# Optimization experiments

Hardware: AMD Instinct MI355X
Metric: run time of the kernel (lower is better)

The kernel has to match this reference:

```python
import jax, jax.numpy as jnp
import numpy as np

N = 50000          # nodes
E = 1_600_000      # edges (avg degree 32)
D_IN = 128
D_H = 128
D_OUT = 64
L = 3              # GATv2 layers
NEG_SLOPE = 0.2    # PyG GATv2Conv default negative_slope


def setup_inputs() -> dict:
    key = jax.random.key(0)
    ks = jax.random.split(key, 12)
    s = 0.05
    x = jax.random.normal(ks[0], (N, D_IN), jnp.float32)
    edge_index = jax.random.randint(ks[1], (2, E), 0, N, jnp.int32)
    # stacked per-layer GATv2 params (input_dim == hidden_dim so all layers match)
    Wl = jax.random.normal(ks[2], (L, D_H, D_H), jnp.float32) * s   # lin_l weights
    bl = jnp.zeros((L, D_H), jnp.float32)
    Wr = jax.random.normal(ks[3], (L, D_H, D_H), jnp.float32) * s   # lin_r weights
    br = jnp.zeros((L, D_H), jnp.float32)
    att = jax.random.normal(ks[4], (L, D_H), jnp.float32) * s       # attention vector a
    bias = jnp.zeros((L, D_H), jnp.float32)                          # post-aggregation bias
    # post_mp MLP head
    W1 = jax.random.normal(ks[5], (D_H, D_H), jnp.float32) * s
    b1 = jnp.zeros((D_H,), jnp.float32)
    W2 = jax.random.normal(ks[6], (D_OUT, D_H), jnp.float32) * s
    b2 = jnp.zeros((D_OUT,), jnp.float32)
    return {"x": x, "edge_index": edge_index, "Wl": Wl, "bl": bl, "Wr": Wr,
            "br": br, "att": att, "bias": bias, "W1": W1, "b1": b1, "W2": W2, "b2": b2}


def _gatv2_layer(x, src, dst, Wl, bl, Wr, br, att, bias):
    # lin_l on source features, lin_r on destination features (heads=1)
    xl = x @ Wl.T + bl                                   # [N, D_H]
    xr = x @ Wr.T + br                                   # [N, D_H]
    e = jax.nn.leaky_relu(xl[src] + xr[dst], NEG_SLOPE)  # [E, D_H]
    logits = e @ att                                     # [E]
    # segment softmax over incoming edges of each destination node
    m = jax.ops.segment_max(logits, dst, num_segments=N)
    ex = jnp.exp(logits - m[dst])
    denom = jax.ops.segment_sum(ex, dst, num_segments=N)
    alpha = ex / denom[dst]                              # [E]
    msg = xl[src] * alpha[:, None]                       # [E, D_H]
    out = jax.ops.segment_sum(msg, dst, num_segments=N)  # [N, D_H]
    return out + bias


def reference(x, edge_index, Wl, bl, Wr, br, att, bias, W1, b1, W2, b2):
    src, dst = edge_index[0], edge_index[1]
    for i in range(L):
        x = _gatv2_layer(x, src, dst, Wl[i], bl[i], Wr[i], br[i], att[i], bias[i])
        x = jax.nn.relu(x)  # dropout is identity in eval mode
    h = x @ W1.T + b1
    return h @ W2.T + b2  # return_embedding=True -> raw output
```

## Files before the change

kernel.cpp:

```cpp
#include <hip/hip_runtime.h>
#include <hip/hip_bf16.h>

#define NN 50000
#define EE 1600000
#define DH 128
#define DOUT 64
#define NEG 0.2f
#define NBK 256
#define CHUNK 4096

typedef short bf16x8 __attribute__((ext_vector_type(8)));
typedef float f32x4 __attribute__((ext_vector_type(4)));


__global__ __launch_bounds__(256) void k_bhist(const int* __restrict__ dst,
                                               int* __restrict__ bucket_hist) {
    __shared__ int lh[NBK];
    lh[threadIdx.x] = 0;
    __syncthreads();
    const int e0 = blockIdx.x * CHUNK;
    #pragma unroll
    for (int k = 0; k < CHUNK / 256; k++) {
        int e = e0 + k * 256 + threadIdx.x;
        if (e < EE) atomicAdd(&lh[((unsigned)dst[e]) >> 8], 1);
    }
    __syncthreads();
    int c = lh[threadIdx.x];
    if (c) atomicAdd(&bucket_hist[threadIdx.x], c);
}

__global__ __launch_bounds__(256) void k_scan_bucket(const int* __restrict__ bucket_hist,
                                                     int* __restrict__ bucket_base,
                                                     int* __restrict__ bucket_cursor) {
    __shared__ int tmp[NBK];
    int t = threadIdx.x;
    int v = bucket_hist[t];
    tmp[t] = v;
    __syncthreads();
    #pragma unroll
    for (int off = 1; off < NBK; off <<= 1) {
        int tt = (t >= off) ? tmp[t - off] : 0;
        __syncthreads();
        tmp[t] += tt;
        __syncthreads();
    }
    bucket_base[t] = tmp[t] - v;
    bucket_cursor[t] = tmp[t] - v;
}

__global__ __launch_bounds__(256) void k_scatter(const int* __restrict__ src,
                                                 const int* __restrict__ dst,
                                                 int* __restrict__ bucket_cursor,
                                                 uint2* __restrict__ pairs) {
    __shared__ int lh[NBK];
    __shared__ int lbase[NBK];
    lh[threadIdx.x] = 0;
    __syncthreads();
    const int e0 = blockIdx.x * CHUNK;
    int dl[CHUNK / 256];
    #pragma unroll
    for (int k = 0; k < CHUNK / 256; k++) {
        int e = e0 + k * 256 + threadIdx.x;
        dl[k] = (e < EE) ? dst[e] : -1;
        if (dl[k] >= 0) atomicAdd(&lh[((unsigned)dl[k]) >> 8], 1);
    }
    __syncthreads();
    int c = lh[threadIdx.x];
    lbase[threadIdx.x] = c ? atomicAdd(&bucket_cursor[threadIdx.x], c) : 0;
    __syncthreads();
    lh[threadIdx.x] = 0;
    __syncthreads();
    #pragma unroll
    for (int k = 0; k < CHUNK / 256; k++) {
        int e = e0 + k * 256 + threadIdx.x;
        if (dl[k] >= 0) {
            int b = ((unsigned)dl[k]) >> 8;
            int loc = atomicAdd(&lh[b], 1);
            pairs[lbase[b] + loc] = make_uint2((unsigned)src[e], (unsigned)dl[k]);
        }
    }
}

__global__ __launch_bounds__(256) void k_bucket(const uint2* __restrict__ pairs,
                                                const int* __restrict__ bucket_base,
                                                const int* __restrict__ bucket_hist,
                                                int* __restrict__ csr_off,
                                                int* __restrict__ prow,
                                                int* __restrict__ deg) {
    __shared__ int cnt[256];
    __shared__ int sbase[256];
    __shared__ int scn[256];
    __shared__ int cur[256];
    const int b = blockIdx.x;
    const int t = threadIdx.x;
    const int pstart = bucket_base[b];
    const int pcnt = bucket_hist[b];

    cnt[t] = 0;
    cur[t] = 0;
    __syncthreads();
    for (int i = t; i < pcnt; i += 256)
        atomicAdd(&cnt[pairs[pstart + i].y & 255u], 1);
    __syncthreads();

    const int d = cnt[t];
    const int padded = (d + 7) & ~7;
    scn[t] = padded;
    __syncthreads();
    #pragma unroll
    for (int off = 1; off < 256; off <<= 1) {
        int v = (t >= off) ? scn[t - off] : 0;
        __syncthreads();
        scn[t] += v;
        __syncthreads();
    }
    const int mybase = scn[t] - padded;
    sbase[t] = mybase;
    const int cb = pstart + b * 2048;
    const int node = b * 256 + t;
    if (node < NN) {
        prow[node] = cb + mybase;
        deg[node] = d;
    }
    __syncthreads();

    for (int i = t; i < pcnt; i += 256) {
        uint2 pr = pairs[pstart + i];
        int ln = (int)(pr.y & 255u);
        int pos = atomicAdd(&cur[ln], 1);
        csr_off[cb + sbase[ln] + pos] = (int)(pr.x << 8);
    }
    __syncthreads();

    for (int p = d; p < padded; p++) csr_off[cb + mybase + p] = 0;
}


static __device__ __forceinline__ unsigned int f2bf(float f) {
    unsigned int u = __float_as_uint(f);
    return (u + 0x7fffu + ((u >> 16) & 1u)) >> 16;
}
static __device__ __forceinline__ unsigned int pack2bf(float lo, float hi) {
    return f2bf(lo) | (f2bf(hi) << 16);
}


template <int BN>
__global__ __launch_bounds__(256) void k_mfma(const float* __restrict__ X,
                                              const float* __restrict__ W0,
                                              const float* __restrict__ b0,
                                              unsigned int* __restrict__ C0bf,
                                              const float* __restrict__ W1,
                                              const float* __restrict__ b1,
                                              float* __restrict__ C1,
                                              int nrows) {
    constexpr int MF = (BN == 128) ? 4 : 2;
    constexpr int NF = 4;
    __shared__ __align__(16) unsigned short As[4][4][128][8];
    __shared__ __align__(16) unsigned short Bs[4][4][BN][8];

    const int tid = threadIdx.x;
    const int row0 = blockIdx.x * 128;
    const bool bfout = (blockIdx.y == 0) && (C0bf != nullptr);
    const float* W = (blockIdx.y == 0) ? W0 : W1;
    const float* bias = (blockIdx.y == 0) ? b0 : b1;

    #pragma unroll
    for (int i = 0; i < 16; i++) {
        int L = i * 256 + tid;
        int r = L >> 5, kq = L & 31;
        int gr = row0 + r;
        float4 v = make_float4(0.f, 0.f, 0.f, 0.f);
        if (gr < nrows) v = *(const float4*)&X[(size_t)gr * 128 + kq * 4];
        int k = kq * 4;
        int kc = k >> 5, kg = (k >> 3) & 3, e = k & 7;
        *(uint2*)&As[kc][kg][r][e] = make_uint2(pack2bf(v.x, v.y), pack2bf(v.z, v.w));
    }
    #pragma unroll
    for (int i = 0; i < (BN * 32) / 256; i++) {
        int L = i * 256 + tid;
        int r = L >> 5, kq = L & 31;
        float4 v = *(const float4*)&W[(size_t)r * 128 + kq * 4];
        int k = kq * 4;
        int kc = k >> 5, kg = (k >> 3) & 3, e = k & 7;
        *(uint2*)&Bs[kc][kg][r][e] = make_uint2(pack2bf(v.x, v.y), pack2bf(v.z, v.w));
    }
    __syncthreads();

    const int w = tid >> 6;
    const int lane = tid & 63;
    const int lr = lane & 15;
    const int kg = lane >> 4;
    const int rowbase = (BN == 128) ? (w >> 1) * 64 : w * 32;
    const int colbase = (BN == 128) ? (w & 1) * 64 : 0;

    f32x4 acc[MF][NF];
    #pragma unroll
    for (int i = 0; i < MF; i++)
        #pragma unroll
        for (int j = 0; j < NF; j++) acc[i][j] = (f32x4){0.f, 0.f, 0.f, 0.f};

    #pragma unroll
    for (int kc = 0; kc < 4; kc++) {
        bf16x8 af[MF], bfr[NF];
        #pragma unroll
        for (int i = 0; i < MF; i++)
            af[i] = *(const bf16x8*)&As[kc][kg][rowbase + i * 16 + lr][0];
        #pragma unroll
        for (int j = 0; j < NF; j++)
            bfr[j] = *(const bf16x8*)&Bs[kc][kg][colbase + j * 16 + lr][0];
        #pragma unroll
        for (int i = 0; i < MF; i++)
            #pragma unroll
            for (int j = 0; j < NF; j++)
                acc[i][j] = __builtin_amdgcn_mfma_f32_16x16x32_bf16(af[i], bfr[j],
                                                                    acc[i][j], 0, 0, 0);
    }

    #pragma unroll
    for (int i = 0; i < MF; i++) {
        #pragma unroll
        for (int reg = 0; reg < 4; reg++) {
            int row = rowbase + i * 16 + (lane >> 4) * 4 + reg;
            int gr = row0 + row;
            if (gr < nrows) {
                #pragma unroll
                for (int j = 0; j < NF; j++) {
                    int col = colbase + j * 16 + lr;
                    float v = acc[i][j][reg] + bias[col];
                    if (bfout) {
                        float vn = __shfl_xor(v, 1, 64);
                        if (!(lane & 1)) {
                            C0bf[(size_t)gr * (BN / 2) + (col >> 1)] = pack2bf(v, vn);
                        }
                    } else {
                        C1[(size_t)gr * BN + col] = v;
                    }
                }
            }
        }
    }
}


__global__ __launch_bounds__(256) void k_gat_node(const unsigned short* __restrict__ xl16,
                                                  const float* __restrict__ xr,
                                                  const float* __restrict__ att,
                                                  const float* __restrict__ bias,
                                                  const int* __restrict__ csr_off,
                                                  const int* __restrict__ prow,
                                                  const int* __restrict__ deg,
                                                  float* __restrict__ xout) {
    const int lane = threadIdx.x & 63;
    const int n = blockIdx.x * 4 + (threadIdx.x >> 6);
    if (n >= NN) return;

    const int l7 = lane & 7;
    const float2 xrv = *(const float2*)&xr[(size_t)n * DH + 2 * lane];
    const float2 attv = *(const float2*)&att[2 * lane];
    const int p0 = prow[n];
    const int dg = deg[n];
    const int pend = p0 + dg;
    const int pend_pad = p0 + ((dg + 7) & ~7);

    float ssum_l = 0.f;
    float ax = 0.f, ay = 0.f;

    const char* xlb = (const char*)xl16;
    const unsigned int lb = (unsigned int)lane * 4u;

    for (int p = p0; p < pend_pad; p += 8) {
        uint4 ia = *(const uint4*)&csr_off[p];
        uint4 ib = *(const uint4*)&csr_off[p + 4];
        unsigned int u0 = *(const unsigned int*)(xlb + (ia.x + lb));
        unsigned int u1 = *(const unsigned int*)(xlb + (ia.y + lb));
        unsigned int u2 = *(const unsigned int*)(xlb + (ia.z + lb));
        unsigned int u3 = *(const unsigned int*)(xlb + (ia.w + lb));
        unsigned int u4 = *(const unsigned int*)(xlb + (ib.x + lb));
        unsigned int u5 = *(const unsigned int*)(xlb + (ib.y + lb));
        unsigned int u6 = *(const unsigned int*)(xlb + (ib.z + lb));
        unsigned int u7 = *(const unsigned int*)(xlb + (ib.w + lb));
        unsigned int uu[8] = {u0, u1, u2, u3, u4, u5, u6, u7};

        float x0[8], x1[8], w[8];
        #pragma unroll
        for (int j = 0; j < 8; j++) {
            x0[j] = __uint_as_float(uu[j] << 16);
            x1[j] = __uint_as_float(uu[j] & 0xffff0000u);
            float z0 = x0[j] + xrv.x;
            float z1 = x1[j] + xrv.y;
            float l0 = fmaxf(z0, NEG * z0);
            float l1 = fmaxf(z1, NEG * z1);
            w[j] = fmaf(l0, attv.x, l1 * attv.y);
        }

        float v4[4], v2[2], S;
        {
            const bool hi = (lane & 1);
            #pragma unroll
            for (int i = 0; i < 4; i++) {
                float keep = hi ? w[2 * i + 1] : w[2 * i];
                float send = hi ? w[2 * i] : w[2 * i + 1];
                v4[i] = keep + __shfl_xor(send, 1, 64);
            }
        }
        {
            const bool hi = (lane & 2);
            #pragma unroll
            for (int i = 0; i < 2; i++) {
                float keep = hi ? v4[2 * i + 1] : v4[2 * i];
                float send = hi ? v4[2 * i] : v4[2 * i + 1];
                v2[i] = keep + __shfl_xor(send, 2, 64);
            }
        }
        {
            const bool hi = (lane & 4);
            float keep = hi ? v2[1] : v2[0];
            float send = hi ? v2[0] : v2[1];
            S = keep + __shfl_xor(send, 4, 64);
        }
        S += __shfl_xor(S, 8, 64);
        S += __shfl_xor(S, 16, 64);
        S += __shfl_xor(S, 32, 64);

        float pe = (p + l7 < pend) ? __expf(S) : 0.f;
        ssum_l += pe;

        float q = __shfl_xor(pe, 1, 64);
        float pA = (l7 & 1) ? q : pe;
        float pB = (l7 & 1) ? pe : q;
        float qA = __shfl_xor(pA, 2, 64);
        float qB = __shfl_xor(pB, 2, 64);
        float p00 = (l7 & 2) ? qA : pA;
        float p01 = (l7 & 2) ? qB : pB;
        float p10 = (l7 & 2) ? pA : qA;
        float p11 = (l7 & 2) ? pB : qB;
        float r00 = __shfl_xor(p00, 4, 64);
        float r01 = __shfl_xor(p01, 4, 64);
        float r10 = __shfl_xor(p10, 4, 64);
        float r11 = __shfl_xor(p11, 4, 64);
        float pe0 = (l7 & 4) ? r00 : p00;
        float pe1 = (l7 & 4) ? r01 : p01;
        float pe2 = (l7 & 4) ? r10 : p10;
        float pe3 = (l7 & 4) ? r11 : p11;
        float pe4 = (l7 & 4) ? p00 : r00;
        float pe5 = (l7 & 4) ? p01 : r01;
        float pe6 = (l7 & 4) ? p10 : r10;
        float pe7 = (l7 & 4) ? p11 : r11;

        ax = fmaf(pe0, x0[0], ax);  ay = fmaf(pe0, x1[0], ay);
        ax = fmaf(pe1, x0[1], ax);  ay = fmaf(pe1, x1[1], ay);
        ax = fmaf(pe2, x0[2], ax);  ay = fmaf(pe2, x1[2], ay);
        ax = fmaf(pe3, x0[3], ax);  ay = fmaf(pe3, x1[3], ay);
        ax = fmaf(pe4, x0[4], ax);  ay = fmaf(pe4, x1[4], ay);
        ax = fmaf(pe5, x0[5], ax);  ay = fmaf(pe5, x1[5], ay);
        ax = fmaf(pe6, x0[6], ax);  ay = fmaf(pe6, x1[6], ay);
        ax = fmaf(pe7, x0[7], ax);  ay = fmaf(pe7, x1[7], ay);
    }

    float st = ssum_l;
    st += __shfl_xor(st, 1, 64);
    st += __shfl_xor(st, 2, 64);
    st += __shfl_xor(st, 4, 64);
    const float inv = (st > 0.f) ? 1.f / st : 0.f;

    const float2 bv = *(const float2*)&bias[2 * lane];
    const float o0 = fmaxf(fmaf(ax, inv, bv.x), 0.f);
    const float o1 = fmaxf(fmaf(ay, inv, bv.y), 0.f);
    *(float2*)&xout[(size_t)n * DH + 2 * lane] = make_float2(o0, o1);
}


static inline size_t align256(size_t x) { return (x + 255) & ~(size_t)255; }

extern "C" void kernel_launch(void* const* d_in, const int* in_sizes, int n_in,
                              void* d_out, int out_size, void* d_ws, size_t ws_size,
                              hipStream_t stream) {
    (void)in_sizes; (void)n_in; (void)out_size; (void)ws_size;

    const float* x   = (const float*)d_in[0];
    const int* ei    = (const int*)d_in[1];
    const float* Wl  = (const float*)d_in[2];
    const float* bl  = (const float*)d_in[3];
    const float* Wr  = (const float*)d_in[4];
    const float* br  = (const float*)d_in[5];
    const float* att = (const float*)d_in[6];
    const float* bias= (const float*)d_in[7];
    const float* W1  = (const float*)d_in[8];
    const float* b1  = (const float*)d_in[9];
    const float* W2  = (const float*)d_in[10];
    const float* b2  = (const float*)d_in[11];
    float* out = (float*)d_out;

    const int* src = ei;
    const int* dst = ei + EE;

    const size_t EP = (size_t)EE + (size_t)NBK * 2048;

    char* w = (char*)d_ws;
    float* xA  = (float*)w; w += align256((size_t)NN * DH * 4);
    float* xB  = (float*)w; w += align256((size_t)NN * DH * 4);
    unsigned int* xl16 = (unsigned int*)w; w += align256((size_t)NN * DH * 2);
    float* xrb = (float*)w; w += align256((size_t)NN * DH * 4);
    float* hbuf = (float*)w; w += align256((size_t)NN * DH * 4);
    uint2* pairs = (uint2*)w; w += align256((size_t)EE * 8);
    int* csr_off = (int*)w; w += align256(EP * 4);
    int* prow    = (int*)w; w += align256((size_t)NN * 4);
    int* deg     = (int*)w; w += align256((size_t)NN * 4);
    int* bucket_hist   = (int*)w; w += align256(NBK * 4);
    int* bucket_base   = (int*)w; w += align256(NBK * 4);
    int* bucket_cursor = (int*)w; w += align256(NBK * 4);

    const int nb_chunk = (EE + CHUNK - 1) / CHUNK;
    const int nb_bkt  = (NN + 255) / 256;
    const int nb_gemm = (NN + 127) / 128;
    const int nb_node = (NN + 3) / 4;

    hipMemsetAsync(bucket_hist, 0, NBK * 4, stream);
    k_bhist<<<nb_chunk, 256, 0, stream>>>(dst, bucket_hist);
    k_scan_bucket<<<1, NBK, 0, stream>>>(bucket_hist, bucket_base, bucket_cursor);
    k_scatter<<<nb_chunk, 256, 0, stream>>>(src, dst, bucket_cursor, pairs);
    k_bucket<<<nb_bkt, 256, 0, stream>>>(pairs, bucket_base, bucket_hist,
                                         csr_off, prow, deg);

    const float* xin = x;
    for (int l = 0; l < 3; ++l) {
        const float* Wl_l = Wl + (size_t)l * DH * DH;
        const float* Wr_l = Wr + (size_t)l * DH * DH;
        const float* bl_l = bl + (size_t)l * DH;
        const float* br_l = br + (size_t)l * DH;
        const float* att_l = att + (size_t)l * DH;
        const float* bias_l = bias + (size_t)l * DH;
        float* xo = (l & 1) ? xB : xA;

        k_mfma<DH><<<dim3(nb_gemm, 2), 256, 0, stream>>>(xin, Wl_l, bl_l, xl16,
                                                         Wr_l, br_l, xrb, NN);
        k_gat_node<<<nb_node, 256, 0, stream>>>((const unsigned short*)xl16, xrb,
                                                att_l, bias_l, csr_off, prow, deg, xo);
        xin = xo;
    }

    k_mfma<DH><<<dim3(nb_gemm, 1), 256, 0, stream>>>(xin, W1, b1, nullptr,
                                                     nullptr, nullptr, hbuf, NN);
    k_mfma<DOUT><<<dim3(nb_gemm, 1), 256, 0, stream>>>(hbuf, W2, b2, nullptr,
                                                       nullptr, nullptr, out, NN);
}
```

Measured before the change: 412.1 us.

## Store layer outputs in bf16, pack edge pairs, fuse MLP head GEMMs

```diff
diff --git a/kernel.cpp b/kernel.cpp
--- a/kernel.cpp
+++ b/kernel.cpp
@@ -51,7 +51,7 @@
 __global__ __launch_bounds__(256) void k_scatter(const int* __restrict__ src,
                                                  const int* __restrict__ dst,
                                                  int* __restrict__ bucket_cursor,
-                                                 uint2* __restrict__ pairs) {
+                                                 unsigned int* __restrict__ pairs) {
     __shared__ int lh[NBK];
     __shared__ int lbase[NBK];
     lh[threadIdx.x] = 0;
@@ -76,12 +76,13 @@
         if (dl[k] >= 0) {
             int b = ((unsigned)dl[k]) >> 8;
             int loc = atomicAdd(&lh[b], 1);
-            pairs[lbase[b] + loc] = make_uint2((unsigned)src[e], (unsigned)dl[k]);
-        }
-    }
-}
-
-__global__ __launch_bounds__(256) void k_bucket(const uint2* __restrict__ pairs,
+            pairs[lbase[b] + loc] =
+                (unsigned)src[e] | (((unsigned)dl[k] & 255u) << 16);
+        }
+    }
+}
+
+__global__ __launch_bounds__(256) void k_bucket(const unsigned int* __restrict__ pairs,
                                                 const int* __restrict__ bucket_base,
                                                 const int* __restrict__ bucket_hist,
                                                 int* __restrict__ csr_off,
@@ -100,7 +101,7 @@
     cur[t] = 0;
     __syncthreads();
     for (int i = t; i < pcnt; i += 256)
-        atomicAdd(&cnt[pairs[pstart + i].y & 255u], 1);
+        atomicAdd(&cnt[pairs[pstart + i] >> 16], 1);
     __syncthreads();
 
     const int d = cnt[t];
@@ -125,10 +126,10 @@
     __syncthreads();
 
     for (int i = t; i < pcnt; i += 256) {
-        uint2 pr = pairs[pstart + i];
-        int ln = (int)(pr.y & 255u);
+        unsigned int pr = pairs[pstart + i];
+        int ln = (int)(pr >> 16);
         int pos = atomicAdd(&cur[ln], 1);
-        csr_off[cb + sbase[ln] + pos] = (int)(pr.x << 8);
+        csr_off[cb + sbase[ln] + pos] = (int)((pr & 0xffffu) << 8);
     }
     __syncthreads();
 
@@ -145,8 +146,8 @@
 }
 
 
-template <int BN>
-__global__ __launch_bounds__(256) void k_mfma(const float* __restrict__ X,
+template <bool ABF>
+__global__ __launch_bounds__(256) void k_mfma(const void* __restrict__ X,
                                               const float* __restrict__ W0,
                                               const float* __restrict__ b0,
                                               unsigned int* __restrict__ C0bf,
@@ -154,27 +155,41 @@
                                               const float* __restrict__ b1,
                                               float* __restrict__ C1,
                                               int nrows) {
-    constexpr int MF = (BN == 128) ? 4 : 2;
-    constexpr int NF = 4;
+    constexpr int BN = 128;
+    constexpr int MF = 4, NF = 4;
     __shared__ __align__(16) unsigned short As[4][4][128][8];
     __shared__ __align__(16) unsigned short Bs[4][4][BN][8];
 
     const int tid = threadIdx.x;
     const int row0 = blockIdx.x * 128;
-    const bool bfout = (blockIdx.y == 0) && (C0bf != nullptr);
-    const float* W = (blockIdx.y == 0) ? W0 : W1;
-    const float* bias = (blockIdx.y == 0) ? b0 : b1;
-
-    #pragma unroll
-    for (int i = 0; i < 16; i++) {
-        int L = i * 256 + tid;
-        int r = L >> 5, kq = L & 31;
-        int gr = row0 + r;
-        float4 v = make_float4(0.f, 0.f, 0.f, 0.f);
-        if (gr < nrows) v = *(const float4*)&X[(size_t)gr * 128 + kq * 4];
-        int k = kq * 4;
-        int kc = k >> 5, kg = (k >> 3) & 3, e = k & 7;
-        *(uint2*)&As[kc][kg][r][e] = make_uint2(pack2bf(v.x, v.y), pack2bf(v.z, v.w));
+    const bool bfout = (blockIdx.y == 0);
+    const float* W = bfout ? W0 : W1;
+    const float* bias = bfout ? b0 : b1;
+
+    if constexpr (ABF) {
+        const uint4* X4 = (const uint4*)X;
+        #pragma unroll
+        for (int i = 0; i < 8; i++) {
+            int L = i * 256 + tid;
+            int r = L >> 4, q = L & 15;
+            int gr = row0 + r;
+            uint4 v = make_uint4(0u, 0u, 0u, 0u);
+            if (gr < nrows) v = X4[(size_t)gr * 16 + q];
+            *(uint4*)&As[q >> 2][q & 3][r][0] = v;
+        }
+    } else {
+        const float* Xf = (const float*)X;
+        #pragma unroll
+        for (int i = 0; i < 16; i++) {
+            int L = i * 256 + tid;
+            int r = L >> 5, kq = L & 31;
+            int gr = row0 + r;
+            float4 v = make_float4(0.f, 0.f, 0.f, 0.f);
+            if (gr < nrows) v = *(const float4*)&Xf[(size_t)gr * 128 + kq * 4];
+            int k = kq * 4;
+            *(uint2*)&As[k >> 5][(k >> 3) & 3][r][k & 7] =
+                make_uint2(pack2bf(v.x, v.y), pack2bf(v.z, v.w));
+        }
     }
     #pragma unroll
     for (int i = 0; i < (BN * 32) / 256; i++) {
@@ -182,8 +197,8 @@
         int r = L >> 5, kq = L & 31;
         float4 v = *(const float4*)&W[(size_t)r * 128 + kq * 4];
         int k = kq * 4;
-        int kc = k >> 5, kg = (k >> 3) & 3, e = k & 7;
-        *(uint2*)&Bs[kc][kg][r][e] = make_uint2(pack2bf(v.x, v.y), pack2bf(v.z, v.w));
+        *(uint2*)&Bs[k >> 5][(k >> 3) & 3][r][k & 7] =
+            make_uint2(pack2bf(v.x, v.y), pack2bf(v.z, v.w));
     }
     __syncthreads();
 
@@ -191,8 +206,8 @@
     const int lane = tid & 63;
     const int lr = lane & 15;
     const int kg = lane >> 4;
-    const int rowbase = (BN == 128) ? (w >> 1) * 64 : w * 32;
-    const int colbase = (BN == 128) ? (w & 1) * 64 : 0;
+    const int rowbase = (w >> 1) * 64;
+    const int colbase = (w & 1) * 64;
 
     f32x4 acc[MF][NF];
     #pragma unroll
@@ -243,6 +258,141 @@
 }
 
 
+__global__ __launch_bounds__(256) void k_head(const void* __restrict__ Xbf,
+                                              const float* __restrict__ W1,
+                                              const float* __restrict__ b1,
+                                              const float* __restrict__ W2,
+                                              const float* __restrict__ b2,
+                                              float* __restrict__ out,
+                                              int nrows) {
+    __shared__ __align__(16) unsigned short As[4][4][128][8];
+    __shared__ __align__(16) unsigned short Bs[4][4][128][8];
+
+    const int tid = threadIdx.x;
+    const int row0 = blockIdx.x * 128;
+
+    const uint4* X4 = (const uint4*)Xbf;
+    #pragma unroll
+    for (int i = 0; i < 8; i++) {
+        int L = i * 256 + tid;
+        int r = L >> 4, q = L & 15;
+        int gr = row0 + r;
+        uint4 v = make_uint4(0u, 0u, 0u, 0u);
+        if (gr < nrows) v = X4[(size_t)gr * 16 + q];
+        *(uint4*)&As[q >> 2][q & 3][r][0] = v;
+    }
+    #pragma unroll
+    for (int i = 0; i < 16; i++) {
+        int L = i * 256 + tid;
+        int r = L >> 5, kq = L & 31;
+        float4 v = *(const float4*)&W1[(size_t)r * 128 + kq * 4];
+        int k = kq * 4;
+        *(uint2*)&Bs[k >> 5][(k >> 3) & 3][r][k & 7] =
+            make_uint2(pack2bf(v.x, v.y), pack2bf(v.z, v.w));
+    }
+    __syncthreads();
+
+    const int w = tid >> 6;
+    const int lane = tid & 63;
+    const int lr = lane & 15;
+    const int kg = lane >> 4;
+    const int rowbase = (w >> 1) * 64;
+    const int colbase = (w & 1) * 64;
+
+    f32x4 acc[4][4];
+    #pragma unroll
+    for (int i = 0; i < 4; i++)
+        #pragma unroll
+        for (int j = 0; j < 4; j++) acc[i][j] = (f32x4){0.f, 0.f, 0.f, 0.f};
+
+    #pragma unroll
+    for (int kc = 0; kc < 4; kc++) {
+        bf16x8 af[4], bfr[4];
+        #pragma unroll
+        for (int i = 0; i < 4; i++)
+            af[i] = *(const bf16x8*)&As[kc][kg][rowbase + i * 16 + lr][0];
+        #pragma unroll
+        for (int j = 0; j < 4; j++)
+            bfr[j] = *(const bf16x8*)&Bs[kc][kg][colbase + j * 16 + lr][0];
+        #pragma unroll
+        for (int i = 0; i < 4; i++)
+            #pragma unroll
+            for (int j = 0; j < 4; j++)
+                acc[i][j] = __builtin_amdgcn_mfma_f32_16x16x32_bf16(af[i], bfr[j],
+                                                                    acc[i][j], 0, 0, 0);
+    }
+    __syncthreads();
+
+    #pragma unroll
+    for (int i = 0; i < 4; i++) {
+        #pragma unroll
+        for (int reg = 0; reg < 4; reg++) {
+            int row = rowbase + i * 16 + (lane >> 4) * 4 + reg;
+            #pragma unroll
+            for (int j = 0; j < 4; j++) {
+                int col = colbase + j * 16 + lr;
+                float v = acc[i][j][reg] + b1[col];
+                float vn = __shfl_xor(v, 1, 64);
+                if (!(lane & 1)) {
+                    *(unsigned int*)&As[col >> 5][(col >> 3) & 3][row][col & 7] =
+                        pack2bf(v, vn);
+                }
+            }
+        }
+    }
+    #pragma unroll
+    for (int i = 0; i < 8; i++) {
+        int L = i * 256 + tid;
+        int r = L >> 5, kq = L & 31;
+        float4 v = *(const float4*)&W2[(size_t)r * 128 + kq * 4];
+        int k = kq * 4;
+        *(uint2*)&Bs[k >> 5][(k >> 3) & 3][r][k & 7] =
+            make_uint2(pack2bf(v.x, v.y), pack2bf(v.z, v.w));
+    }
+    __syncthreads();
+
+    const int rowbase2 = w * 32;
+    f32x4 acc2[2][4];
+    #pragma unroll
+    for (int i = 0; i < 2; i++)
+        #pragma unroll
+        for (int j = 0; j < 4; j++) acc2[i][j] = (f32x4){0.f, 0.f, 0.f, 0.f};
+
+    #pragma unroll
+    for (int kc = 0; kc < 4; kc++) {
+        bf16x8 af2[2], bf2[4];
+        #pragma unroll
+        for (int i = 0; i < 2; i++)
+            af2[i] = *(const bf16x8*)&As[kc][kg][rowbase2 + i * 16 + lr][0];
+        #pragma unroll
+        for (int j = 0; j < 4; j++)
+            bf2[j] = *(const bf16x8*)&Bs[kc][kg][j * 16 + lr][0];
+        #pragma unroll
+        for (int i = 0; i < 2; i++)
+            #pragma unroll
+            for (int j = 0; j < 4; j++)
+                acc2[i][j] = __builtin_amdgcn_mfma_f32_16x16x32_bf16(af2[i], bf2[j],
+                                                                     acc2[i][j], 0, 0, 0);
+    }
+
+    #pragma unroll
+    for (int i = 0; i < 2; i++) {
+        #pragma unroll
+        for (int reg = 0; reg < 4; reg++) {
+            int row = rowbase2 + i * 16 + (lane >> 4) * 4 + reg;
+            int gr = row0 + row;
+            if (gr < nrows) {
+                #pragma unroll
+                for (int j = 0; j < 4; j++) {
+                    int col = j * 16 + lr;
+                    out[(size_t)gr * DOUT + col] = acc2[i][j][reg] + b2[col];
+                }
+            }
+        }
+    }
+}
+
+
 __global__ __launch_bounds__(256) void k_gat_node(const unsigned short* __restrict__ xl16,
                                                   const float* __restrict__ xr,
                                                   const float* __restrict__ att,
@@ -250,7 +400,7 @@
                                                   const int* __restrict__ csr_off,
                                                   const int* __restrict__ prow,
                                                   const int* __restrict__ deg,
-                                                  float* __restrict__ xout) {
+                                                  unsigned int* __restrict__ xout) {
     const int lane = threadIdx.x & 63;
     const int n = blockIdx.x * 4 + (threadIdx.x >> 6);
     if (n >= NN) return;
@@ -367,7 +517,7 @@
     const float2 bv = *(const float2*)&bias[2 * lane];
     const float o0 = fmaxf(fmaf(ax, inv, bv.x), 0.f);
     const float o1 = fmaxf(fmaf(ay, inv, bv.y), 0.f);
-    *(float2*)&xout[(size_t)n * DH + 2 * lane] = make_float2(o0, o1);
+    xout[(size_t)n * (DH / 2) + lane] = pack2bf(o0, o1);
 }
 
 
@@ -398,12 +548,11 @@
     const size_t EP = (size_t)EE + (size_t)NBK * 2048;
 
     char* w = (char*)d_ws;
-    float* xA  = (float*)w; w += align256((size_t)NN * DH * 4);
-    float* xB  = (float*)w; w += align256((size_t)NN * DH * 4);
+    unsigned int* xA = (unsigned int*)w; w += align256((size_t)NN * (DH / 2) * 4);
+    unsigned int* xB = (unsigned int*)w; w += align256((size_t)NN * (DH / 2) * 4);
     unsigned int* xl16 = (unsigned int*)w; w += align256((size_t)NN * DH * 2);
     float* xrb = (float*)w; w += align256((size_t)NN * DH * 4);
-    float* hbuf = (float*)w; w += align256((size_t)NN * DH * 4);
-    uint2* pairs = (uint2*)w; w += align256((size_t)EE * 8);
+    unsigned int* pairs = (unsigned int*)w; w += align256((size_t)EE * 4);
     int* csr_off = (int*)w; w += align256(EP * 4);
     int* prow    = (int*)w; w += align256((size_t)NN * 4);
     int* deg     = (int*)w; w += align256((size_t)NN * 4);
@@ -423,7 +572,7 @@
     k_bucket<<<nb_bkt, 256, 0, stream>>>(pairs, bucket_base, bucket_hist,
                                          csr_off, prow, deg);
 
-    const float* xin = x;
+    const void* xin = (const void*)x;
     for (int l = 0; l < 3; ++l) {
         const float* Wl_l = Wl + (size_t)l * DH * DH;
         const float* Wr_l = Wr + (size_t)l * DH * DH;
@@ -431,17 +580,18 @@
         const float* br_l = br + (size_t)l * DH;
         const float* att_l = att + (size_t)l * DH;
         const float* bias_l = bias + (size_t)l * DH;
-        float* xo = (l & 1) ? xB : xA;
-
-        k_mfma<DH><<<dim3(nb_gemm, 2), 256, 0, stream>>>(xin, Wl_l, bl_l, xl16,
-                                                         Wr_l, br_l, xrb, NN);
+        unsigned int* xo = (l & 1) ? xB : xA;
+
+        if (l == 0)
+            k_mfma<false><<<dim3(nb_gemm, 2), 256, 0, stream>>>(xin, Wl_l, bl_l, xl16,
+                                                                Wr_l, br_l, xrb, NN);
+        else
+            k_mfma<true><<<dim3(nb_gemm, 2), 256, 0, stream>>>(xin, Wl_l, bl_l, xl16,
+                                                               Wr_l, br_l, xrb, NN);
         k_gat_node<<<nb_node, 256, 0, stream>>>((const unsigned short*)xl16, xrb,
                                                 att_l, bias_l, csr_off, prow, deg, xo);
-        xin = xo;
-    }
-
-    k_mfma<DH><<<dim3(nb_gemm, 1), 256, 0, stream>>>(xin, W1, b1, nullptr,
-                                                     nullptr, nullptr, hbuf, NN);
-    k_mfma<DOUT><<<dim3(nb_gemm, 1), 256, 0, stream>>>(hbuf, W2, b2, nullptr,
-                                                       nullptr, nullptr, out, NN);
-}
+        xin = (const void*)xo;
+    }
+
+    k_head<<<nb_gemm, 256, 0, stream>>>(xin, W1, b1, W2, b2, out, NN);
+}
```

After: 381.4 us. 1.08x faster.
